# Optimization experiments

Hardware: AMD Instinct MI355X
Metric: run time of the kernel (lower is better)

## Reference

```python
import jax, jax.numpy as jnp
import numpy as np
from jax import lax

NPOINT, RADIUS, NSAMPLE = 1024, 0.2, 32
POS_CH = 3
BN_EPS = 1e-5


def farthest_point_sample(xyz, m):
    # xyz: (b, n, 3) -> idx (b, m); matches pointops: start at index 0,
    # iteratively pick argmax of running min-distance-to-selected-set.
    b, n, _ = xyz.shape

    def step(carry, _):
        temp, far = carry                                   # temp (b,n), far (b,)
        cur = jnp.take_along_axis(xyz, far[:, None, None], axis=1)  # (b,1,3)
        d = jnp.sum((xyz - cur) ** 2, axis=-1)              # (b,n)
        temp = jnp.minimum(temp, d)
        nxt = jnp.argmax(temp, axis=-1).astype(jnp.int32)
        return (temp, nxt), far

    init = (jnp.full((b, n), 1e10, xyz.dtype), jnp.zeros((b,), jnp.int32))
    _, idx = lax.scan(step, init, None, length=m)
    return idx.T                                            # (b, m)


def query_ball_point(radius, nsample, xyz, new_xyz):
    # For each query, the first `nsample` point indices with d2 < r^2 (ascending
    # index order, like the CUDA kernel); short lists padded with the first hit;
    # empty balls -> index 0 (zero-init semantics of pointops).
    n = xyz.shape[1]
    d2 = jnp.sum((new_xyz[:, :, None, :] - xyz[:, None, :, :]) ** 2, axis=-1)  # (b,m,n)
    cand = jnp.where(d2 < radius * radius, jnp.arange(n, dtype=jnp.int32), n)
    neg, _ = lax.top_k(-cand, nsample)                      # k smallest indices
    idx = -neg                                              # (b,m,nsample)
    first = idx[:, :, :1]
    idx = jnp.where(idx == n, jnp.where(first == n, 0, first), idx)
    return idx


def gather_points(pts, idx):
    # pts (b,n,c), idx (b,m) -> (b,m,c)
    return jnp.take_along_axis(pts, idx[..., None], axis=1)


def group_points(pts, idx):
    # pts (b,n,c), idx (b,m,ns) -> (b,m,ns,c)
    b, m, ns = idx.shape
    g = jnp.take_along_axis(pts, idx.reshape(b, m * ns)[..., None], axis=1)
    return g.reshape(b, m, ns, -1)


def conv1x1(x, w, b):
    # x (b,c,s,m), w (o,c), b (o,)
    return jnp.einsum('bcsm,oc->bosm', x, w) + b[None, :, None, None]


def batch_norm(x, g, be):
    # training-mode BatchNorm2d over (b, s, m) per channel, biased variance
    mu = jnp.mean(x, axis=(0, 2, 3), keepdims=True)
    var = jnp.var(x, axis=(0, 2, 3), keepdims=True)
    xn = (x - mu) * lax.rsqrt(var + BN_EPS)
    return g[None, :, None, None] * xn + be[None, :, None, None]


def _forward(center, normal, feature,
             w_l0, b_l0, g_l0, be_l0, w_f0, b_f0, g_f0, be_f0,
             w1, b1, g1, be1, w2, b2, g2, be2):
    feat = jnp.transpose(feature, (0, 2, 1))                # (b,n,C)

    fps_idx = lax.stop_gradient(farthest_point_sample(center, NPOINT))  # (b,m)
    new_center = gather_points(center, fps_idx)             # (b,m,3)
    new_normal = gather_points(normal, fps_idx)             # (b,m,3)

    idx = lax.stop_gradient(
        query_ball_point(RADIUS, NSAMPLE, center, lax.stop_gradient(new_center)))

    group_normal = group_points(normal, idx)                # (b,m,ns,3)
    group_center = group_points(center, idx)                # (b,m,ns,3)
    group_center_norm = group_center - new_center[:, :, None, :]
    group_feature = group_points(feat, idx)                 # (b,m,ns,C)

    new_feature = jnp.concatenate(
        [group_center_norm, group_normal, group_feature], axis=-1)  # (b,m,ns,12)
    x = jnp.transpose(new_feature, (0, 3, 2, 1))            # (b,12,ns,m)

    loc = batch_norm(conv1x1(x[:, :POS_CH], w_l0, b_l0), g_l0, be_l0)
    ftr = batch_norm(conv1x1(x[:, POS_CH:], w_f0, b_f0), g_f0, be_f0)
    x = jax.nn.relu(loc + ftr)
    x = jax.nn.relu(batch_norm(conv1x1(x, w1, b1), g1, be1))
    x = jax.nn.relu(batch_norm(conv1x1(x, w2, b2), g2, be2))
    x = jnp.max(x, axis=2)                                  # (b,128,m)

    return (jnp.transpose(new_center, (0, 2, 1)),
            jnp.transpose(new_normal, (0, 2, 1)),
            x)


def setup_inputs() -> dict:
    key = jax.random.key(0)
    ks = jax.random.split(key, 16)
    B, N, CF = 8, 8192, 6
    inp = {
        'center': jax.random.uniform(ks[0], (B, N, 3), jnp.float32),
        'normal': jax.random.normal(ks[1], (B, N, 3), jnp.float32),
        'feature': jax.random.normal(ks[2], (B, CF, N), jnp.float32),
        'w_l0': jax.random.normal(ks[3], (64, 3), jnp.float32) * 0.1,
        'b_l0': jax.random.normal(ks[4], (64,), jnp.float32) * 0.05,
        'g_l0': jnp.ones((64,), jnp.float32),
        'be_l0': jnp.zeros((64,), jnp.float32),
        'w_f0': jax.random.normal(ks[5], (64, 9), jnp.float32) * 0.1,
        'b_f0': jax.random.normal(ks[6], (64,), jnp.float32) * 0.05,
        'g_f0': jnp.ones((64,), jnp.float32),
        'be_f0': jnp.zeros((64,), jnp.float32),
        'w1': jax.random.normal(ks[7], (64, 64), jnp.float32) * 0.1,
        'b1': jax.random.normal(ks[8], (64,), jnp.float32) * 0.05,
        'g1': jnp.ones((64,), jnp.float32),
        'be1': jnp.zeros((64,), jnp.float32),
        'w2': jax.random.normal(ks[9], (128, 64), jnp.float32) * 0.1,
        'b2': jax.random.normal(ks[10], (128,), jnp.float32) * 0.05,
        'g2': jnp.ones((128,), jnp.float32),
        'be2': jnp.zeros((128,), jnp.float32),
    }
    return inp


def reference(center, normal, feature,
              w_l0, b_l0, g_l0, be_l0, w_f0, b_f0, g_f0, be_f0,
              w1, b1, g1, be1, w2, b2, g2, be2):
    return _forward(center, normal, feature,
                    w_l0, b_l0, g_l0, be_l0, w_f0, b_f0, g_f0, be_f0,
                    w1, b1, g1, be1, w2, b2, g2, be2)
```

## Files before the change

kernel.cpp:

```cpp
#include <hip/hip_runtime.h>
#include <hip/hip_bf16.h>
#include <cstdint>
#include <cstddef>

#define BB 8
#define NN 8192
#define MM 1024
#define SS 32
#define PTOT (BB*MM*SS)
__device__ __constant__ float kR2 = 0.039999999105930328f;

#define ST_SUM0L 0
#define ST_SQ0L  64
#define ST_SUM0F 128
#define ST_SQ0F  192
#define ST_SUM1  256
#define ST_SQ1   320
#define ST_SUM2  384
#define ST_SQ2   512
#define P_AL     640
#define P_BL     704
#define P_AF     768
#define P_BF     832
#define P_A1     896
#define P_B1     960
#define P_A2     1024
#define P_B2     1152
#define STATS_ZERO_BYTES (640*4)

#define OFF_FPS   0u
#define OFF_STATS 32768u
#define OFF_X0    40960u
#define OFF_Z1    12623872u

typedef float v2f __attribute__((ext_vector_type(2)));

__global__ __launch_bounds__(512, 2) void fps_kernel(const float* __restrict__ center,
                                                     int* __restrict__ fps_idx) {
  const int b = blockIdx.x;
  const int t = threadIdx.x;
  const int lane = t & 63, wid = t >> 6;
  const float* cb = center + (size_t)b * NN * 3;
  __shared__ __align__(16) float4 sc[NN];
  __shared__ unsigned long long s_wkey[2][8];
  v2f X[8], Y[8], Z[8], T[8];
#pragma unroll
  for (int j = 0; j < 8; ++j) {
    const int p0 = ((2 * j) << 9) | t;
    const int p1 = ((2 * j + 1) << 9) | t;
    const float x0 = cb[p0 * 3 + 0], y0 = cb[p0 * 3 + 1], z0 = cb[p0 * 3 + 2];
    const float x1 = cb[p1 * 3 + 0], y1 = cb[p1 * 3 + 1], z1 = cb[p1 * 3 + 2];
    sc[p0] = make_float4(x0, y0, z0, 0.f);
    sc[p1] = make_float4(x1, y1, z1, 0.f);
    X[j] = (v2f){x0, x1}; Y[j] = (v2f){y0, y1}; Z[j] = (v2f){z0, z1};
    T[j] = (v2f){1e10f, 1e10f};
    asm volatile("" : "+v"(X[j]), "+v"(Y[j]), "+v"(Z[j]));
  }
  __syncthreads();
  int far = 0;
  for (int i = 0; i < MM; ++i) {
    if (t == 0) fps_idx[(b << 10) + i] = far;
    const float4 c = sc[__builtin_amdgcn_readfirstlane(far)];
    const v2f cx2 = (v2f){c.x, c.x};
    const v2f cy2 = (v2f){c.y, c.y};
    const v2f cz2 = (v2f){c.z, c.z};
    {
#pragma clang fp contract(off)
#pragma unroll
      for (int j = 0; j < 8; ++j) {
        const v2f dx = X[j] - cx2;
        const v2f dy = Y[j] - cy2;
        const v2f dz = Z[j] - cz2;
        v2f d = dx * dx;
        d = d + dy * dy;
        d = d + dz * dz;
        T[j].x = fminf(T[j].x, d.x);
        T[j].y = fminf(T[j].y, d.y);
      }
    }
    const float a0 = fmaxf(T[0].x, T[0].y), a1 = fmaxf(T[1].x, T[1].y);
    const float a2 = fmaxf(T[2].x, T[2].y), a3 = fmaxf(T[3].x, T[3].y);
    const float a4 = fmaxf(T[4].x, T[4].y), a5 = fmaxf(T[5].x, T[5].y);
    const float a6 = fmaxf(T[6].x, T[6].y), a7 = fmaxf(T[7].x, T[7].y);
    const float b0 = fmaxf(a0, a1), b1 = fmaxf(a2, a3);
    const float b2 = fmaxf(a4, a5), b3 = fmaxf(a6, a7);
    const float c0 = fmaxf(b0, b1), c1 = fmaxf(b2, b3);
    const float lmax = fmaxf(c0, c1);
    int lidx = 0x7fffffff;
#pragma unroll
    for (int j = 7; j >= 0; --j) {
      if (T[j].y == lmax) lidx = ((2 * j + 1) << 9) | t;
      if (T[j].x == lmax) lidx = ((2 * j) << 9) | t;
    }
    unsigned long long key =
        ((unsigned long long)__float_as_uint(lmax) << 32) | (unsigned)(~lidx);
    for (int off = 1; off < 64; off <<= 1) {
      const unsigned long long ok = __shfl_xor(key, off);
      key = (ok > key) ? ok : key;
    }
    if (lane == 0) s_wkey[i & 1][wid] = key;
    __syncthreads();
    const unsigned long long* sk = s_wkey[i & 1];
    unsigned long long best = sk[0];
#pragma unroll
    for (int w = 1; w < 8; ++w) { const unsigned long long o = sk[w]; best = (o > best) ? o : best; }
    far = (int)(~(unsigned)best);
  }
}

__global__ __launch_bounds__(256) void ball_gather_kernel(
    const float* __restrict__ center, const float* __restrict__ normal,
    const float* __restrict__ feature, const int* __restrict__ fps_idx,
    float* __restrict__ x0, float* __restrict__ out) {
  const int lane = threadIdx.x & 63;
  const int wq = (int)((blockIdx.x * blockDim.x + threadIdx.x) >> 6);
  const int b = wq >> 10, m = wq & 1023;
  const float* cb = center  + (size_t)b * NN * 3;
  const float* nb = normal  + (size_t)b * NN * 3;
  const float* fb = feature + (size_t)b * 6 * NN;
  const int pstar = fps_idx[(b << 10) + m];
  const float qx = cb[pstar * 3 + 0], qy = cb[pstar * 3 + 1], qz = cb[pstar * 3 + 2];
  if (lane < 3) {
    out[b * 3072 + lane * 1024 + m]         = cb[pstar * 3 + lane];
    out[24576 + b * 3072 + lane * 1024 + m] = nb[pstar * 3 + lane];
  }
  const size_t pos_base = (size_t)((b << 10) + m) * SS;
  int total = 0;
  int first_p = -1;
  const float r2 = kR2;
  for (int base = 0; base < NN && total < SS; base += 64) {
    const int p = base + lane;
    const float ppx = cb[p * 3], ppy = cb[p * 3 + 1], ppz = cb[p * 3 + 2];
    const float dx = ppx - qx, dy = ppy - qy, dz = ppz - qz;
    float d2;
    {
#pragma clang fp contract(off)
      d2 = dx * dx;
      d2 = d2 + dy * dy;
      d2 = d2 + dz * dz;
    }
    const bool hit = d2 < r2;
    const unsigned long long msk = __ballot(hit);
    if (first_p < 0 && msk) first_p = base + (int)__builtin_ctzll(msk);
    const int rank = (int)__popcll(msk & ((1ull << lane) - 1ull));
    const int slot = total + rank;
    if (hit && slot < SS) {
      float4 v0, v1, v2;
      v0.x = dx; v0.y = dy; v0.z = dz;
      v0.w = nb[p * 3 + 0];
      v1.x = nb[p * 3 + 1];
      v1.y = nb[p * 3 + 2];
      v1.z = fb[p];
      v1.w = fb[NN + p];
      v2.x = fb[2 * NN + p];
      v2.y = fb[3 * NN + p];
      v2.z = fb[4 * NN + p];
      v2.w = fb[5 * NN + p];
      float4* dst = (float4*)(x0 + (pos_base + (size_t)slot) * 12);
      dst[0] = v0; dst[1] = v1; dst[2] = v2;
    }
    total += (int)__popcll(msk);
  }
  if (total < SS) {
    if (first_p < 0) first_p = 0;
    const int p = first_p;
    const float ppx = cb[p * 3], ppy = cb[p * 3 + 1], ppz = cb[p * 3 + 2];
    float4 v0, v1, v2;
    v0.x = ppx - qx; v0.y = ppy - qy; v0.z = ppz - qz;
    v0.w = nb[p * 3 + 0]; v1.x = nb[p * 3 + 1]; v1.y = nb[p * 3 + 2];
    v1.z = fb[p]; v1.w = fb[NN + p];
    v2.x = fb[2 * NN + p]; v2.y = fb[3 * NN + p]; v2.z = fb[4 * NN + p]; v2.w = fb[5 * NN + p];
    for (int slot = total + lane; slot < SS; slot += 64) {
      float4* dst = (float4*)(x0 + (pos_base + (size_t)slot) * 12);
      dst[0] = v0; dst[1] = v1; dst[2] = v2;
    }
  }
}

__global__ __launch_bounds__(256) void stats0_kernel(
    const float* __restrict__ x0,
    const float* __restrict__ w_l0, const float* __restrict__ b_l0,
    const float* __restrict__ w_f0, const float* __restrict__ b_f0,
    float* __restrict__ stats) {
  const int lane = threadIdx.x & 63, wid = threadIdx.x >> 6;
  const int wgid = blockIdx.x * 4 + wid;
  float wl[3], wf[9];
#pragma unroll
  for (int j = 0; j < 3; ++j) wl[j] = w_l0[lane * 3 + j];
#pragma unroll
  for (int j = 0; j < 9; ++j) wf[j] = w_f0[lane * 9 + j];
  const float bl = b_l0[lane], bf = b_f0[lane];
  float sL = 0.f, qL = 0.f, sF = 0.f, qF = 0.f;
  for (int it = 0; it < 128; ++it) {
    const int p = it * 2048 + wgid;
    const float4* row = (const float4*)(x0 + (size_t)p * 12);
    const float4 r0 = row[0], r1 = row[1], r2 = row[2];
    const float yL = bl + wl[0] * r0.x + wl[1] * r0.y + wl[2] * r0.z;
    const float yF = bf + wf[0] * r0.w + wf[1] * r1.x + wf[2] * r1.y + wf[3] * r1.z +
                     wf[4] * r1.w + wf[5] * r2.x + wf[6] * r2.y + wf[7] * r2.z + wf[8] * r2.w;
    sL += yL; qL += yL * yL; sF += yF; qF += yF * yF;
  }
  __shared__ float red[4][64][4];
  red[wid][lane][0] = sL; red[wid][lane][1] = qL;
  red[wid][lane][2] = sF; red[wid][lane][3] = qF;
  __syncthreads();
  if (wid == 0) {
    float a0 = 0.f, a1 = 0.f, a2 = 0.f, a3 = 0.f;
    for (int w = 0; w < 4; ++w) {
      a0 += red[w][lane][0]; a1 += red[w][lane][1];
      a2 += red[w][lane][2]; a3 += red[w][lane][3];
    }
    atomicAdd(&stats[ST_SUM0L + lane], a0);
    atomicAdd(&stats[ST_SQ0L + lane], a1);
    atomicAdd(&stats[ST_SUM0F + lane], a2);
    atomicAdd(&stats[ST_SQ0F + lane], a3);
  }
}

__global__ void finalize0_kernel(float* stats, const float* gl, const float* bel,
                                 const float* gf, const float* bef) {
  const int t = threadIdx.x;
  const float invN = 1.0f / (float)PTOT;
  if (t < 64) {
    const float mean = stats[ST_SUM0L + t] * invN;
    const float var  = stats[ST_SQ0L + t] * invN - mean * mean;
    const float a = gl[t] / sqrtf(var + 1e-5f);
    stats[P_AL + t] = a;
    stats[P_BL + t] = bel[t] - a * mean;
  } else {
    const int c = t - 64;
    const float mean = stats[ST_SUM0F + c] * invN;
    const float var  = stats[ST_SQ0F + c] * invN - mean * mean;
    const float a = gf[c] / sqrtf(var + 1e-5f);
    stats[P_AF + c] = a;
    stats[P_BF + c] = bef[c] - a * mean;
  }
}
__global__ void finalize1_kernel(float* stats, const float* g, const float* be) {
  const int t = threadIdx.x;
  const float invN = 1.0f / (float)PTOT;
  const float mean = stats[ST_SUM1 + t] * invN;
  const float var  = stats[ST_SQ1 + t] * invN - mean * mean;
  const float a = g[t] / sqrtf(var + 1e-5f);
  stats[P_A1 + t] = a;
  stats[P_B1 + t] = be[t] - a * mean;
}
__global__ void finalize2_kernel(float* stats, const float* g, const float* be) {
  const int t = threadIdx.x;
  const float invN = 1.0f / (float)PTOT;
  const float mean = stats[ST_SUM2 + t] * invN;
  const float var  = stats[ST_SQ2 + t] * invN - mean * mean;
  const float a = g[t] / sqrtf(var + 1e-5f);
  stats[P_A2 + t] = a;
  stats[P_B2 + t] = be[t] - a * mean;
}

__global__ __launch_bounds__(256) void k5_kernel(
    const float* __restrict__ x0, float* __restrict__ z1,
    float* __restrict__ stats,
    const float* __restrict__ w_l0, const float* __restrict__ b_l0,
    const float* __restrict__ w_f0, const float* __restrict__ b_f0,
    const float* __restrict__ w1, const float* __restrict__ b1) {
  const int lane = threadIdx.x & 63, wid = threadIdx.x >> 6;
  const int wgid = blockIdx.x * 4 + wid;
  float wl[3], wf[9], w1r[64];
#pragma unroll
  for (int j = 0; j < 3; ++j) wl[j] = w_l0[lane * 3 + j];
#pragma unroll
  for (int j = 0; j < 9; ++j) wf[j] = w_f0[lane * 9 + j];
#pragma unroll
  for (int k = 0; k < 64; ++k) w1r[k] = w1[lane * 64 + k];
  const float bl = b_l0[lane], bf = b_f0[lane], b1v = b1[lane];
  const float aL = stats[P_AL + lane], bL = stats[P_BL + lane];
  const float aF = stats[P_AF + lane], bF = stats[P_BF + lane];
  float s1 = 0.f, q1 = 0.f;
  __shared__ __align__(16) float sx[2][4][64];
  for (int it = 0; it < 128; ++it) {
    const int p = it * 2048 + wgid;
    const float4* row = (const float4*)(x0 + (size_t)p * 12);
    const float4 r0 = row[0], r1 = row[1], r2 = row[2];
    const float yL = bl + wl[0] * r0.x + wl[1] * r0.y + wl[2] * r0.z;
    const float yF = bf + wf[0] * r0.w + wf[1] * r1.x + wf[2] * r1.y + wf[3] * r1.z +
                     wf[4] * r1.w + wf[5] * r2.x + wf[6] * r2.y + wf[7] * r2.z + wf[8] * r2.w;
    const float x1 = fmaxf(aL * yL + bL + (aF * yF + bF), 0.f);
    sx[it & 1][wid][lane] = x1;
    __syncthreads();
    float acc = b1v;
    const float4* xv = (const float4*)&sx[it & 1][wid][0];
#pragma unroll
    for (int k4 = 0; k4 < 16; ++k4) {
      const float4 xq = xv[k4];
      acc += w1r[4 * k4 + 0] * xq.x + w1r[4 * k4 + 1] * xq.y +
             w1r[4 * k4 + 2] * xq.z + w1r[4 * k4 + 3] * xq.w;
    }
    s1 += acc; q1 += acc * acc;
    z1[(size_t)p * 64 + lane] = acc;
  }
  __shared__ float red[4][64][2];
  red[wid][lane][0] = s1; red[wid][lane][1] = q1;
  __syncthreads();
  if (wid == 0) {
    float a0 = 0.f, a1v = 0.f;
    for (int w = 0; w < 4; ++w) { a0 += red[w][lane][0]; a1v += red[w][lane][1]; }
    atomicAdd(&stats[ST_SUM1 + lane], a0);
    atomicAdd(&stats[ST_SQ1 + lane], a1v);
  }
}

__global__ __launch_bounds__(256, 2) void k6_kernel(
    float* __restrict__ z12, float* __restrict__ stats,
    const float* __restrict__ w2, const float* __restrict__ b2) {
  const int lane = threadIdx.x & 63, wid = threadIdx.x >> 6;
  const int wgid = blockIdx.x * 4 + wid;
  float w2a[64], w2b[64];
#pragma unroll
  for (int k = 0; k < 64; ++k) w2a[k] = w2[lane * 64 + k];
#pragma unroll
  for (int k = 0; k < 64; ++k) w2b[k] = w2[(lane + 64) * 64 + k];
  const float b2a = b2[lane], b2b = b2[lane + 64];
  const float a1 = stats[P_A1 + lane], b1p = stats[P_B1 + lane];
  float s0 = 0.f, q0 = 0.f, s1 = 0.f, q1 = 0.f;
  __shared__ __align__(16) float sx[2][4][64];
  __hip_bfloat16* zo = (__hip_bfloat16*)z12;
  for (int it = 0; it < 128; ++it) {
    const int p = it * 2048 + wgid;
    const float z = z12[(size_t)p * 64 + lane];
    const float x2 = fmaxf(a1 * z + b1p, 0.f);
    sx[it & 1][wid][lane] = x2;
    __syncthreads();
    float acc0 = b2a, acc1 = b2b;
    const float4* xv = (const float4*)&sx[it & 1][wid][0];
#pragma unroll
    for (int k4 = 0; k4 < 16; ++k4) {
      const float4 xq = xv[k4];
      acc0 += w2a[4 * k4] * xq.x + w2a[4 * k4 + 1] * xq.y + w2a[4 * k4 + 2] * xq.z + w2a[4 * k4 + 3] * xq.w;
      acc1 += w2b[4 * k4] * xq.x + w2b[4 * k4 + 1] * xq.y + w2b[4 * k4 + 2] * xq.z + w2b[4 * k4 + 3] * xq.w;
    }
    s0 += acc0; q0 += acc0 * acc0; s1 += acc1; q1 += acc1 * acc1;
    zo[(size_t)p * 128 + lane]      = __float2bfloat16(acc0);
    zo[(size_t)p * 128 + 64 + lane] = __float2bfloat16(acc1);
  }
  __shared__ float red[4][64][4];
  red[wid][lane][0] = s0; red[wid][lane][1] = q0;
  red[wid][lane][2] = s1; red[wid][lane][3] = q1;
  __syncthreads();
  if (wid == 0) {
    float t0 = 0.f, t1 = 0.f, t2 = 0.f, t3 = 0.f;
    for (int w = 0; w < 4; ++w) {
      t0 += red[w][lane][0]; t1 += red[w][lane][1];
      t2 += red[w][lane][2]; t3 += red[w][lane][3];
    }
    atomicAdd(&stats[ST_SUM2 + lane], t0);
    atomicAdd(&stats[ST_SQ2 + lane], t1);
    atomicAdd(&stats[ST_SUM2 + 64 + lane], t2);
    atomicAdd(&stats[ST_SQ2 + 64 + lane], t3);
  }
}

__global__ __launch_bounds__(256) void k7_kernel(const __hip_bfloat16* __restrict__ z2,
                                                 const float* __restrict__ stats,
                                                 float* __restrict__ out3) {
  const int b = blockIdx.x >> 4;
  const int mt = blockIdx.x & 15;
  const int t = threadIdx.x;
  const int o = t & 127, h = t >> 7;
  const float a = stats[P_A2 + o], bb = stats[P_B2 + o];
  __shared__ float tile[128][65];
  for (int j = 0; j < 32; ++j) {
    const int ml = h + 2 * j;
    const size_t rowbase = ((size_t)(b * 1024 + mt * 64 + ml)) * SS;
    float acc = -1e30f;
    for (int s = 0; s < SS; ++s) {
      const float v = __bfloat162float(z2[(rowbase + s) * 128 + o]);
      acc = fmaxf(acc, a * v + bb);
    }
    tile[o][ml] = fmaxf(acc, 0.f);
  }
  __syncthreads();
  const int r = t >> 1, c0 = (t & 1) * 32;
  float* dst = out3 + (size_t)b * 128 * 1024 + (size_t)r * 1024 + mt * 64 + c0;
  for (int j = 0; j < 32; ++j) dst[j] = tile[r][c0 + j];
}

extern "C" void kernel_launch(void* const* d_in, const int* in_sizes, int n_in,
                              void* d_out, int out_size, void* d_ws, size_t ws_size,
                              hipStream_t stream) {
  const float* center  = (const float*)d_in[0];
  const float* normal  = (const float*)d_in[1];
  const float* feature = (const float*)d_in[2];
  const float* w_l0 = (const float*)d_in[3];
  const float* b_l0 = (const float*)d_in[4];
  const float* g_l0 = (const float*)d_in[5];
  const float* be_l0 = (const float*)d_in[6];
  const float* w_f0 = (const float*)d_in[7];
  const float* b_f0 = (const float*)d_in[8];
  const float* g_f0 = (const float*)d_in[9];
  const float* be_f0 = (const float*)d_in[10];
  const float* w1 = (const float*)d_in[11];
  const float* b1 = (const float*)d_in[12];
  const float* g1 = (const float*)d_in[13];
  const float* be1 = (const float*)d_in[14];
  const float* w2 = (const float*)d_in[15];
  const float* b2 = (const float*)d_in[16];
  const float* g2 = (const float*)d_in[17];
  const float* be2 = (const float*)d_in[18];
  float* out = (float*)d_out;
  char* ws = (char*)d_ws;
  int*   fps_idx = (int*)(ws + OFF_FPS);
  float* stats   = (float*)(ws + OFF_STATS);
  float* x0      = (float*)(ws + OFF_X0);
  float* z1      = (float*)(ws + OFF_Z1);

  hipMemsetAsync(stats, 0, STATS_ZERO_BYTES, stream);
  hipLaunchKernelGGL(fps_kernel, dim3(8), dim3(512), 0, stream, center, fps_idx);
  hipLaunchKernelGGL(ball_gather_kernel, dim3(2048), dim3(256), 0, stream,
                     center, normal, feature, fps_idx, x0, out);
  hipLaunchKernelGGL(stats0_kernel, dim3(512), dim3(256), 0, stream,
                     x0, w_l0, b_l0, w_f0, b_f0, stats);
  hipLaunchKernelGGL(finalize0_kernel, dim3(1), dim3(128), 0, stream,
                     stats, g_l0, be_l0, g_f0, be_f0);
  hipLaunchKernelGGL(k5_kernel, dim3(512), dim3(256), 0, stream,
                     x0, z1, stats, w_l0, b_l0, w_f0, b_f0, w1, b1);
  hipLaunchKernelGGL(finalize1_kernel, dim3(1), dim3(64), 0, stream, stats, g1, be1);
  hipLaunchKernelGGL(k6_kernel, dim3(512), dim3(256), 0, stream, z1, stats, w2, b2);
  hipLaunchKernelGGL(finalize2_kernel, dim3(1), dim3(128), 0, stream, stats, g2, be2);
  hipLaunchKernelGGL(k7_kernel, dim3(128), dim3(256), 0, stream,
                     (const __hip_bfloat16*)z1, stats, out + 49152);
}
```

Baseline: 1.503 ms.

## Restructure FPS argmax with 256-thread blocks, packed keys and DPP reductions

The farthest-point-sampling kernel now runs 256 threads per block, each holding 32 points in registers instead of 16. This halves the number of waves that sync each iteration and shortens the cross-wave reduction to 4 entries. The per-thread argmax now builds packed (distance bits, inverted index) 64-bit keys and reduces them with a compare tree, replacing the max-then-search scan. The wave-level reduction uses DPP row operations instead of shuffle-xor. Each thread now does twice the serial distance work per iteration and uses more registers, in exchange for cheaper reduction and synchronisation.

```diff
diff --git a/kernel.cpp b/kernel.cpp
--- a/kernel.cpp
+++ b/kernel.cpp
@@ -34,20 +34,31 @@
 #define OFF_Z1    12623872u
 
 typedef float v2f __attribute__((ext_vector_type(2)));
-
-__global__ __launch_bounds__(512, 2) void fps_kernel(const float* __restrict__ center,
+typedef unsigned long long ull;
+
+#define DPP_KMAX(k, ctrl, rm, bm) {                                        \
+  const unsigned _lo = (unsigned)(k), _hi = (unsigned)((k) >> 32);         \
+  const unsigned _nl = (unsigned)__builtin_amdgcn_update_dpp(              \
+      (int)_lo, (int)_lo, ctrl, rm, bm, false);                            \
+  const unsigned _nh = (unsigned)__builtin_amdgcn_update_dpp(              \
+      (int)_hi, (int)_hi, ctrl, rm, bm, false);                            \
+  const ull _o = ((ull)_nh << 32) | _nl;                                   \
+  k = (_o > (k)) ? _o : (k); }
+
+__global__ __launch_bounds__(256, 1) void fps_kernel(const float* __restrict__ center,
                                                      int* __restrict__ fps_idx) {
   const int b = blockIdx.x;
   const int t = threadIdx.x;
   const int lane = t & 63, wid = t >> 6;
   const float* cb = center + (size_t)b * NN * 3;
   __shared__ __align__(16) float4 sc[NN];
-  __shared__ unsigned long long s_wkey[2][8];
-  v2f X[8], Y[8], Z[8], T[8];
-#pragma unroll
-  for (int j = 0; j < 8; ++j) {
-    const int p0 = ((2 * j) << 9) | t;
-    const int p1 = ((2 * j + 1) << 9) | t;
+  __shared__ ull s_wkey[2][4];
+  v2f X[16], Y[16], Z[16], T[16];
+  unsigned nidx[32];
+#pragma unroll
+  for (int j = 0; j < 16; ++j) {
+    const int p0 = ((2 * j) << 8) | t;
+    const int p1 = ((2 * j + 1) << 8) | t;
     const float x0 = cb[p0 * 3 + 0], y0 = cb[p0 * 3 + 1], z0 = cb[p0 * 3 + 2];
     const float x1 = cb[p1 * 3 + 0], y1 = cb[p1 * 3 + 1], z1 = cb[p1 * 3 + 2];
     sc[p0] = make_float4(x0, y0, z0, 0.f);
@@ -56,6 +67,8 @@
     T[j] = (v2f){1e10f, 1e10f};
     asm volatile("" : "+v"(X[j]), "+v"(Y[j]), "+v"(Z[j]));
   }
+#pragma unroll
+  for (int k = 0; k < 32; ++k) nidx[k] = ~(unsigned)((k << 8) | t);
   __syncthreads();
   int far = 0;
   for (int i = 0; i < MM; ++i) {
@@ -67,43 +80,48 @@
     {
 #pragma clang fp contract(off)
 #pragma unroll
-      for (int j = 0; j < 8; ++j) {
+      for (int j = 0; j < 16; ++j) {
         const v2f dx = X[j] - cx2;
         const v2f dy = Y[j] - cy2;
         const v2f dz = Z[j] - cz2;
         v2f d = dx * dx;
         d = d + dy * dy;
         d = d + dz * dz;
-        T[j].x = fminf(T[j].x, d.x);
-        T[j].y = fminf(T[j].y, d.y);
+        T[j] = __builtin_elementwise_min(T[j], d);
       }
     }
-    const float a0 = fmaxf(T[0].x, T[0].y), a1 = fmaxf(T[1].x, T[1].y);
-    const float a2 = fmaxf(T[2].x, T[2].y), a3 = fmaxf(T[3].x, T[3].y);
-    const float a4 = fmaxf(T[4].x, T[4].y), a5 = fmaxf(T[5].x, T[5].y);
-    const float a6 = fmaxf(T[6].x, T[6].y), a7 = fmaxf(T[7].x, T[7].y);
-    const float b0 = fmaxf(a0, a1), b1 = fmaxf(a2, a3);
-    const float b2 = fmaxf(a4, a5), b3 = fmaxf(a6, a7);
-    const float c0 = fmaxf(b0, b1), c1 = fmaxf(b2, b3);
-    const float lmax = fmaxf(c0, c1);
-    int lidx = 0x7fffffff;
-#pragma unroll
-    for (int j = 7; j >= 0; --j) {
-      if (T[j].y == lmax) lidx = ((2 * j + 1) << 9) | t;
-      if (T[j].x == lmax) lidx = ((2 * j) << 9) | t;
-    }
-    unsigned long long key =
-        ((unsigned long long)__float_as_uint(lmax) << 32) | (unsigned)(~lidx);
-    for (int off = 1; off < 64; off <<= 1) {
-      const unsigned long long ok = __shfl_xor(key, off);
-      key = (ok > key) ? ok : key;
-    }
-    if (lane == 0) s_wkey[i & 1][wid] = key;
+    ull K[16];
+#pragma unroll
+    for (int j = 0; j < 16; ++j) {
+      const unsigned hx = __float_as_uint(T[j].x);
+      const unsigned hy = __float_as_uint(T[j].y);
+      const bool ygt = hy > hx;
+      const unsigned h = ygt ? hy : hx;
+      const unsigned l = ygt ? nidx[2 * j + 1] : nidx[2 * j];
+      K[j] = ((ull)h << 32) | l;
+    }
+#pragma unroll
+    for (int s = 8; s >= 1; s >>= 1) {
+#pragma unroll
+      for (int j = 0; j < s; ++j) {
+        const ull o = K[j + s];
+        if (o > K[j]) K[j] = o;
+      }
+    }
+    ull key = K[0];
+    DPP_KMAX(key, 0x111, 0xf, 0xf)
+    DPP_KMAX(key, 0x112, 0xf, 0xf)
+    DPP_KMAX(key, 0x114, 0xf, 0xe)
+    DPP_KMAX(key, 0x118, 0xf, 0xc)
+    DPP_KMAX(key, 0x142, 0xa, 0xf)
+    DPP_KMAX(key, 0x143, 0xc, 0xf)
+    if (lane == 63) s_wkey[i & 1][wid] = key;
     __syncthreads();
-    const unsigned long long* sk = s_wkey[i & 1];
-    unsigned long long best = sk[0];
-#pragma unroll
-    for (int w = 1; w < 8; ++w) { const unsigned long long o = sk[w]; best = (o > best) ? o : best; }
+    const ull* sk = s_wkey[i & 1];
+    const ull k0 = sk[0], k1 = sk[1], k2 = sk[2], k3 = sk[3];
+    const ull h0 = (k1 > k0) ? k1 : k0;
+    const ull h1 = (k3 > k2) ? k3 : k2;
+    const ull best = (h1 > h0) ? h1 : h0;
     far = (int)(~(unsigned)best);
   }
 }
@@ -412,7 +430,7 @@
   float* z1      = (float*)(ws + OFF_Z1);
 
   hipMemsetAsync(stats, 0, STATS_ZERO_BYTES, stream);
-  hipLaunchKernelGGL(fps_kernel, dim3(8), dim3(512), 0, stream, center, fps_idx);
+  hipLaunchKernelGGL(fps_kernel, dim3(8), dim3(256), 0, stream, center, fps_idx);
   hipLaunchKernelGGL(ball_gather_kernel, dim3(2048), dim3(256), 0, stream,
                      center, normal, feature, fps_idx, x0, out);
   hipLaunchKernelGGL(stats0_kernel, dim3(512), dim3(256), 0, stream,
```

After: 1.308 ms. -13.0%, faster.
